# Optimization experiments

Measured on AMD Instinct MI355X. Metric: run time of the kernel, lower is better.

## Reference

```python
import jax, jax.numpy as jnp
import numpy as np

SEQ_LEN = 64  # config.SEQ_LEN
T, B, N, D = 256, 128, 4, 2
H_HIS, H_INT = 32, 8


def _uniform(key, shape, k):
    return jax.random.uniform(key, shape, jnp.float32, -k, k)


def setup_inputs() -> dict:
    key = jax.random.key(0)
    ks = jax.random.split(key, 12)
    kh = 1.0 / np.sqrt(H_HIS)
    ki = 1.0 / np.sqrt(H_INT)
    ko = 1.0 / np.sqrt(40)
    return {
        "inputs": jax.random.normal(ks[0], (T, B, N, D), jnp.float32),
        # history LSTM (input 2 -> hidden 32), gate order i,f,g,o like torch
        "Wih_his": _uniform(ks[1], (4 * H_HIS, D), kh),
        "Whh_his": _uniform(ks[2], (4 * H_HIS, H_HIS), kh),
        "bih_his": _uniform(ks[3], (4 * H_HIS,), kh),
        "bhh_his": _uniform(ks[4], (4 * H_HIS,), kh),
        # interaction LSTM (input 2 -> hidden 8)
        "Wih_int": _uniform(ks[5], (4 * H_INT, D), ki),
        "Whh_int": _uniform(ks[6], (4 * H_INT, H_INT), ki),
        "bih_int": _uniform(ks[7], (4 * H_INT,), ki),
        "bhh_int": _uniform(ks[8], (4 * H_INT,), ki),
        # output Linear(40 -> 2)
        "W_out": _uniform(ks[9], (2, H_HIS + H_INT), ko),
        "b_out": _uniform(ks[10], (2,), ko),
    }


def _lstm_windows(x_w, valid, Wih, Whh, bih, bhh):
    """Run an LSTM over L steps for T independent windows at once.
    x_w: [L, Tw, B, d]  inputs per step (leading padding for short windows)
    valid: [L, Tw] bool; while False the state is held at zero, which is
    exactly equivalent to starting the window fresh at its first valid step.
    Returns final hidden state h: [Tw, B, H].
    """
    H = Whh.shape[1]
    Tw, Bb = x_w.shape[1], x_w.shape[2]
    b = bih + bhh

    def step(carry, xs):
        h, c = carry
        x, v = xs
        g = x @ Wih.T + h @ Whh.T + b            # [Tw, B, 4H]
        i, f, gg, o = jnp.split(g, 4, axis=-1)
        c_new = jax.nn.sigmoid(f) * c + jax.nn.sigmoid(i) * jnp.tanh(gg)
        h_new = jax.nn.sigmoid(o) * jnp.tanh(c_new)
        m = v[:, None, None]
        return (jnp.where(m, h_new, 0.0), jnp.where(m, c_new, 0.0)), None

    init = (jnp.zeros((Tw, Bb, H), x_w.dtype), jnp.zeros((Tw, Bb, H), x_w.dtype))
    (h, _), _ = jax.lax.scan(step, init, (x_w, valid))
    return h


def reference(inputs, Wih_his, Whh_his, bih_his, bhh_his,
              Wih_int, Whh_int, bih_int, bhh_int, W_out, b_out):
    Tt, Bb, Nn, Dd = inputs.shape
    L = SEQ_LEN
    # window index for output frame t: frames t-L+1 .. t (clipped; invalid masked)
    t = jnp.arange(Tt)[:, None]
    s = jnp.arange(L)[None, :]
    idx = t - (L - 1) + s                      # [T, L]
    valid = (idx >= 0)
    idx_c = jnp.clip(idx, 0, Tt - 1)
    x_his = inputs[:, :, -1, :][idx_c]         # [T, L, B, d] (ego / last node)
    x_int = inputs[:, :, 0, :][idx_c]          # [T, L, B, d] (interaction node)
    x_his = jnp.transpose(x_his, (1, 0, 2, 3))  # [L, T, B, d]
    x_int = jnp.transpose(x_int, (1, 0, 2, 3))
    v = jnp.transpose(valid)                   # [L, T]

    h_his = _lstm_windows(x_his, v, Wih_his, Whh_his, bih_his, bhh_his)  # [T,B,32]
    h_int = _lstm_windows(x_int, v, Wih_int, Whh_int, bih_int, bhh_int)  # [T,B,8]
    emb = jnp.concatenate([h_his, h_int], axis=-1)                       # [T,B,40]
    return emb @ W_out.T + b_out                                         # [T,B,2]
```

## Files before the change

kernel.cpp:

```cpp
#include <hip/hip_runtime.h>


typedef float v2f __attribute__((ext_vector_type(2)));
typedef float v4f __attribute__((ext_vector_type(4)));
typedef _Float16 h8v __attribute__((ext_vector_type(8)));

static __device__ __forceinline__ float fexp2(float x) {
    return __builtin_amdgcn_exp2f(x);
}
static __device__ __forceinline__ float frcp(float x) {
    return __builtin_amdgcn_rcpf(x);
}
static __device__ __forceinline__ void pk_fma(v2f& d, v2f a, v2f b) {
    asm("v_pk_fma_f32 %0, %1, %2, %0" : "+v"(d) : "v"(a), "v"(b));
}
static __device__ __forceinline__ v2f loh(v4f v) {
    return __builtin_shufflevector(v, v, 0, 1);
}
static __device__ __forceinline__ v2f hih(v4f v) {
    return __builtin_shufflevector(v, v, 2, 3);
}
static __device__ __forceinline__ unsigned short f2h(float f) {
    _Float16 h = (_Float16)f;
    unsigned short u;
    __builtin_memcpy(&u, &h, 2);
    return u;
}

#define LOG2E    1.442695041f
#define TWOLOG2E 2.885390082f

__global__ __launch_bounds__(256) void prep_kernel(
    const float* __restrict__ Wih_his, const float* __restrict__ Whh_his,
    const float* __restrict__ bih_his, const float* __restrict__ bhh_his,
    const float* __restrict__ Wih_int, const float* __restrict__ Whh_int,
    const float* __restrict__ bih_int, const float* __restrict__ bhh_int,
    float* __restrict__ ws)
{
    const int i = blockIdx.x * 256 + threadIdx.x;
    if (i < 4480) {
        if (i < 256) {
            const int r = i >> 1;
            const float s = (r >= 64 && r < 96) ? -TWOLOG2E : -LOG2E;
            ws[i] = Wih_his[i] * s;
        } else if (i < 384) {
            const int r = i - 256;
            const float s = (r >= 64 && r < 96) ? -TWOLOG2E : -LOG2E;
            ws[i] = (bih_his[r] + bhh_his[r]) * s;
        } else {
            const int e = i - 384, r = e >> 5;
            const float s = (r >= 64 && r < 96) ? -TWOLOG2E : -LOG2E;
            ws[i] = Whh_his[e] * s;
        }
    } else if (i < 4544) {
        const int e = i - 4480, r = e >> 1;
        const float s = (r >= 16 && r < 24) ? -TWOLOG2E : -LOG2E;
        ws[i] = Wih_int[e] * s;
    } else if (i < 4576) {
        const int r = i - 4544;
        const float s = (r >= 16 && r < 24) ? -TWOLOG2E : -LOG2E;
        ws[i] = (bih_int[r] + bhh_int[r]) * s;
    } else if (i < 4832) {
        const int e = i - 4576, r = e >> 3;
        const float s = (r >= 16 && r < 24) ? -TWOLOG2E : -LOG2E;
        ws[i] = Whh_int[e] * s;
    } else if (i < 4960) {
        const int p = i - 4832;
        const int T = p >> 4, n = p & 15;
        const int gi = T >> 1, u = 2 * n + (T & 1);
        const int r = gi * 32 + u;
        const float s = (gi == 2) ? -TWOLOG2E : -LOG2E;
        ws[5120 + p] = (bih_his[r] + bhh_his[r]) * s;
    } else if (i < 5216) {
        const int e = i - 4960;
        const int p = e >> 1, comp = e & 1;
        const int T = p >> 4, n = p & 15;
        const int gi = T >> 1, u = 2 * n + (T & 1);
        const int r = gi * 32 + u;
        const float s = (gi == 2) ? -TWOLOG2E : -LOG2E;
        ws[5376 + e] = Wih_his[r * 2 + comp] * s;
    } else if (i < 9312) {
        const int e = i - 5216;
        const int p = e >> 5, k = e & 31;
        const int T = p >> 4, n = p & 15;
        const int gi = T >> 1, u = 2 * n + (T & 1);
        const int r = gi * 32 + u;
        const float s = (gi == 2) ? -TWOLOG2E : -LOG2E;
        reinterpret_cast<unsigned short*>(ws)[11776 + e] =
            f2h(Whh_his[r * 32 + k] * s);
    }
}

__global__ __launch_bounds__(64) void int_kernel(
    const float* __restrict__ inp, const float* __restrict__ ws,
    const float* __restrict__ W_out, float* __restrict__ eInt)
{
    __shared__ __align__(16) float ib[2][8][8];

    const int lane = threadIdx.x;
    const int W    = blockIdx.x;
    const int t    = W >> 4;
    const int g    = lane >> 3;
    const int u    = lane & 7;
    const int b    = ((W & 15) << 3) | g;
    const int nsteps = (t >= 63) ? 64 : (t + 1);
    const int tau0   = (t >= 63) ? (t - 63) : 0;

    v2f wi[4][4], wxi[4];
    float bi[4];
    {
        const v2f* wsWi = reinterpret_cast<const v2f*>(ws + 4576);
        const v2f* wsXi = reinterpret_cast<const v2f*>(ws + 4480);
#pragma unroll
        for (int q = 0; q < 4; ++q) {
            const v2f* row = wsWi + (q * 8 + u) * 4;
#pragma unroll
            for (int k = 0; k < 4; ++k) wi[q][k] = row[k];
            bi[q]  = ws[4544 + q * 8 + u];
            wxi[q] = wsXi[q * 8 + u];
        }
    }

    ib[0][g][u] = 0.f;
    float cc = 0.f, h = 0.f;

    const float* xc = inp + tau0 * 1024 + b * 8;
    float2 xv2 = *reinterpret_cast<const float2*>(xc);
    xc += 1024;

#pragma unroll 1
    for (int s = 0; s < nsteps; ++s) {
        __builtin_amdgcn_wave_barrier();
        asm volatile("s_waitcnt lgkmcnt(0)" ::: "memory");
        __builtin_amdgcn_wave_barrier();

        const int rb = s & 1, wb = rb ^ 1;
        const v4f* ip = reinterpret_cast<const v4f*>(&ib[rb][g][0]);
        const v4f i0 = ip[0], i1 = ip[1];

        float2 nx = {0.f, 0.f};
        if (s + 1 < nsteps) nx = *reinterpret_cast<const float2*>(xc);
        xc += 1024;
        const v2f xv = {xv2.x, xv2.y};

        float a[4];
#pragma unroll
        for (int q = 0; q < 4; ++q) {
            v2f acc = {bi[q], 0.f};
            pk_fma(acc, wxi[q], xv);
            pk_fma(acc, wi[q][0], loh(i0));
            pk_fma(acc, wi[q][1], hih(i0));
            pk_fma(acc, wi[q][2], loh(i1));
            pk_fma(acc, wi[q][3], hih(i1));
            a[q] = acc.x + acc.y;
        }
        const float si = frcp(1.f + fexp2(a[0]));
        const float sf = frcp(1.f + fexp2(a[1]));
        const float tg = fmaf(2.f, frcp(1.f + fexp2(a[2])), -1.f);
        const float so = frcp(1.f + fexp2(a[3]));
        cc = fmaf(sf, cc, si * tg);
        h = so * fmaf(-2.f, frcp(1.f + fexp2(TWOLOG2E * cc)), 1.f);
        ib[wb][g][u] = h;

        xv2 = nx;
    }

    float e0 = W_out[32 + u] * h;
    float e1 = W_out[72 + u] * h;
#pragma unroll
    for (int m = 4; m >= 1; m >>= 1) {
        e0 += __shfl_xor(e0, m);
        e1 += __shfl_xor(e1, m);
    }
    if (u == 0) {
        float2 o; o.x = e0; o.y = e1;
        reinterpret_cast<float2*>(eInt)[t * 128 + b] = o;
    }
}

__global__ __launch_bounds__(64) void his_kernel(
    const float* __restrict__ inp, const float* __restrict__ ws,
    const float* __restrict__ W_out, const float* __restrict__ b_out,
    const float* __restrict__ eInt, float* __restrict__ out)
{
    __shared__ __align__(16) unsigned short hm[2][16][40];

    const int lane = threadIdx.x;
    const int n    = lane & 15;
    const int quad = lane >> 4;
    const int Wd   = blockIdx.x;
    const int t    = Wd >> 3;
    const int bg   = Wd & 7;
    const int nsteps = (t >= 63) ? 64 : (t + 1);
    const int tau0   = (t >= 63) ? (t - 63) : 0;

    h8v Bf[8];
    {
        const h8v* wb = reinterpret_cast<const h8v*>(
            reinterpret_cast<const unsigned short*>(ws) + 11776);
#pragma unroll
        for (int T = 0; T < 8; ++T) Bf[T] = wb[(T * 16 + n) * 4 + quad];
    }
    float cb[8], cw0[8], cw1[8];
#pragma unroll
    for (int T = 0; T < 8; ++T) {
        const int p = T * 16 + n;
        cb[T]  = ws[5120 + p];
        cw0[T] = ws[5376 + 2 * p];
        cw1[T] = ws[5376 + 2 * p + 1];
    }

    const int bbase = bg * 16 + quad * 4;
    const float* xp = inp + tau0 * 1024 + bbase * 8 + 6;
    float2 xc[4];
#pragma unroll
    for (int r = 0; r < 4; ++r)
        xc[r] = *reinterpret_cast<const float2*>(xp + r * 8);
    xp += 1024;

    h8v Af = {};
    float cs[4][2] = {};
    float h0[4] = {}, h1[4] = {};

#pragma unroll 1
    for (int s = 0; s < nsteps; ++s) {
        float2 xn[4];
        if (s + 1 < nsteps) {
#pragma unroll
            for (int r = 0; r < 4; ++r)
                xn[r] = *reinterpret_cast<const float2*>(xp + r * 8);
        } else {
#pragma unroll
            for (int r = 0; r < 4; ++r) xn[r] = make_float2(0.f, 0.f);
        }
        xp += 1024;

        v4f D[8];
#pragma unroll
        for (int T = 0; T < 8; ++T) {
            v4f C;
#pragma unroll
            for (int r = 0; r < 4; ++r)
                C[r] = fmaf(cw1[T], xc[r].y, fmaf(cw0[T], xc[r].x, cb[T]));
            D[T] = __builtin_amdgcn_mfma_f32_16x16x32_f16(Af, Bf[T], C, 0, 0, 0);
        }

#pragma unroll
        for (int r = 0; r < 4; ++r) {
            {
                const float si = frcp(1.f + fexp2(D[0][r]));
                const float sf = frcp(1.f + fexp2(D[2][r]));
                const float tg = fmaf(2.f, frcp(1.f + fexp2(D[4][r])), -1.f);
                const float so = frcp(1.f + fexp2(D[6][r]));
                const float cn = fmaf(sf, cs[r][0], si * tg);
                cs[r][0] = cn;
                h0[r] = so * fmaf(-2.f, frcp(1.f + fexp2(TWOLOG2E * cn)), 1.f);
            }
            {
                const float si = frcp(1.f + fexp2(D[1][r]));
                const float sf = frcp(1.f + fexp2(D[3][r]));
                const float tg = fmaf(2.f, frcp(1.f + fexp2(D[5][r])), -1.f);
                const float so = frcp(1.f + fexp2(D[7][r]));
                const float cn = fmaf(sf, cs[r][1], si * tg);
                cs[r][1] = cn;
                h1[r] = so * fmaf(-2.f, frcp(1.f + fexp2(TWOLOG2E * cn)), 1.f);
            }
        }

        if (s + 1 < nsteps) {
            const int bf = s & 1;
#pragma unroll
            for (int r = 0; r < 4; ++r) {
                const unsigned pk =
                    ((unsigned)f2h(h1[r]) << 16) | f2h(h0[r]);
                *reinterpret_cast<unsigned*>(&hm[bf][quad * 4 + r][2 * n]) = pk;
            }
            __builtin_amdgcn_wave_barrier();
            asm volatile("s_waitcnt lgkmcnt(0)" ::: "memory");
            __builtin_amdgcn_wave_barrier();
            Af = *reinterpret_cast<const h8v*>(&hm[bf][n][quad * 8]);
        }

#pragma unroll
        for (int r = 0; r < 4; ++r) xc[r] = xn[r];
    }

    const float wo0a = W_out[2 * n],      wo0b = W_out[2 * n + 1];
    const float wo1a = W_out[40 + 2 * n], wo1b = W_out[40 + 2 * n + 1];
    float e0[4], e1[4];
#pragma unroll
    for (int r = 0; r < 4; ++r) {
        e0[r] = fmaf(wo0b, h1[r], wo0a * h0[r]);
        e1[r] = fmaf(wo1b, h1[r], wo1a * h0[r]);
#pragma unroll
        for (int m = 1; m <= 8; m <<= 1) {
            e0[r] += __shfl_xor(e0[r], m);
            e1[r] += __shfl_xor(e1[r], m);
        }
    }
    if (n == 0) {
        const float bo0 = b_out[0], bo1 = b_out[1];
#pragma unroll
        for (int r = 0; r < 4; ++r) {
            const int chain = t * 128 + bbase + r;
            const float2 ei = reinterpret_cast<const float2*>(eInt)[chain];
            float2 o;
            o.x = e0[r] + ei.x + bo0;
            o.y = e1[r] + ei.y + bo1;
            reinterpret_cast<float2*>(out)[chain] = o;
        }
    }
}

extern "C" void kernel_launch(void* const* d_in, const int* in_sizes, int n_in,
                              void* d_out, int out_size, void* d_ws, size_t ws_size,
                              hipStream_t stream) {
    const float* inp     = (const float*)d_in[0];
    const float* Wih_his = (const float*)d_in[1];
    const float* Whh_his = (const float*)d_in[2];
    const float* bih_his = (const float*)d_in[3];
    const float* bhh_his = (const float*)d_in[4];
    const float* Wih_int = (const float*)d_in[5];
    const float* Whh_int = (const float*)d_in[6];
    const float* bih_int = (const float*)d_in[7];
    const float* bhh_int = (const float*)d_in[8];
    const float* W_out   = (const float*)d_in[9];
    const float* b_out   = (const float*)d_in[10];
    float* out  = (float*)d_out;
    float* ws   = (float*)d_ws;
    float* eInt = ws + 8192;

    prep_kernel<<<dim3(37), dim3(256), 0, stream>>>(
        Wih_his, Whh_his, bih_his, bhh_his,
        Wih_int, Whh_int, bih_int, bhh_int, ws);

    int_kernel<<<dim3(4096), dim3(64), 0, stream>>>(inp, ws, W_out, eInt);

    his_kernel<<<dim3(2048), dim3(64), 0, stream>>>(
        inp, ws, W_out, b_out, eInt, out);
}
```

Before: 210.3 us.

## Fuse interaction and history LSTM kernels into one launch with atomic output accumulation

Merges the separate interaction and history LSTM kernels into a single kernel that interleaves block types (one history block per two interaction blocks). The prep kernel now initializes the output with the bias, and both branches accumulate their partial projections into the output with atomicAdd instead of going through an intermediate eInt buffer. This removes a kernel launch and its serialization, and lets the two workloads overlap on the GPU. In exchange it adds atomics and makes the result order-dependent, so float rounding may vary between runs.

```diff
diff --git a/kernel.cpp b/kernel.cpp
--- a/kernel.cpp
+++ b/kernel.cpp
@@ -35,7 +35,8 @@
     const float* __restrict__ bih_his, const float* __restrict__ bhh_his,
     const float* __restrict__ Wih_int, const float* __restrict__ Whh_int,
     const float* __restrict__ bih_int, const float* __restrict__ bhh_int,
-    float* __restrict__ ws)
+    float* __restrict__ ws, const float* __restrict__ b_out,
+    float* __restrict__ out)
 {
     const int i = blockIdx.x * 256 + threadIdx.x;
     if (i < 4480) {
@@ -88,17 +89,21 @@
         const float s = (gi == 2) ? -TWOLOG2E : -LOG2E;
         reinterpret_cast<unsigned short*>(ws)[11776 + e] =
             f2h(Whh_his[r * 32 + k] * s);
-    }
-}
-
-__global__ __launch_bounds__(64) void int_kernel(
+    } else if (i >= 9472) {
+        const int j = i - 9472;
+        float4 v;
+        v.x = b_out[0]; v.y = b_out[1];
+        v.z = b_out[0]; v.w = b_out[1];
+        reinterpret_cast<float4*>(out)[j] = v;
+    }
+}
+
+static __device__ __forceinline__ void int_body(
+    const int W, const int lane,
     const float* __restrict__ inp, const float* __restrict__ ws,
-    const float* __restrict__ W_out, float* __restrict__ eInt)
+    const float* __restrict__ W_out, float* __restrict__ out,
+    float ib[2][8][8])
 {
-    __shared__ __align__(16) float ib[2][8][8];
-
-    const int lane = threadIdx.x;
-    const int W    = blockIdx.x;
     const int t    = W >> 4;
     const int g    = lane >> 3;
     const int u    = lane & 7;
@@ -173,22 +178,20 @@
         e1 += __shfl_xor(e1, m);
     }
     if (u == 0) {
-        float2 o; o.x = e0; o.y = e1;
-        reinterpret_cast<float2*>(eInt)[t * 128 + b] = o;
-    }
-}
-
-__global__ __launch_bounds__(64) void his_kernel(
+        const int chain = t * 128 + b;
+        atomicAdd(&out[2 * chain],     e0);
+        atomicAdd(&out[2 * chain + 1], e1);
+    }
+}
+
+static __device__ __forceinline__ void his_body(
+    const int Wd, const int lane,
     const float* __restrict__ inp, const float* __restrict__ ws,
-    const float* __restrict__ W_out, const float* __restrict__ b_out,
-    const float* __restrict__ eInt, float* __restrict__ out)
+    const float* __restrict__ W_out, float* __restrict__ out,
+    unsigned short hm[2][16][40])
 {
-    __shared__ __align__(16) unsigned short hm[2][16][40];
-
-    const int lane = threadIdx.x;
     const int n    = lane & 15;
     const int quad = lane >> 4;
-    const int Wd   = blockIdx.x;
     const int t    = Wd >> 3;
     const int bg   = Wd & 7;
     const int nsteps = (t >= 63) ? 64 : (t + 1);
@@ -299,16 +302,29 @@
         }
     }
     if (n == 0) {
-        const float bo0 = b_out[0], bo1 = b_out[1];
 #pragma unroll
         for (int r = 0; r < 4; ++r) {
             const int chain = t * 128 + bbase + r;
-            const float2 ei = reinterpret_cast<const float2*>(eInt)[chain];
-            float2 o;
-            o.x = e0[r] + ei.x + bo0;
-            o.y = e1[r] + ei.y + bo1;
-            reinterpret_cast<float2*>(out)[chain] = o;
-        }
+            atomicAdd(&out[2 * chain],     e0[r]);
+            atomicAdd(&out[2 * chain + 1], e1[r]);
+        }
+    }
+}
+
+__global__ __launch_bounds__(64) void lstm_fused(
+    const float* __restrict__ inp, const float* __restrict__ ws,
+    const float* __restrict__ W_out, float* __restrict__ out)
+{
+    __shared__ __align__(16) unsigned short hm[2][16][40];
+    __shared__ __align__(16) float ib[2][8][8];
+
+    const int bid  = blockIdx.x;
+    const int lane = threadIdx.x;
+    const int d3   = bid / 3;
+    if (bid - 3 * d3 == 0) {
+        his_body(d3, lane, inp, ws, W_out, out, hm);
+    } else {
+        int_body(bid - d3 - 1, lane, inp, ws, W_out, out, ib);
     }
 }
 
@@ -328,14 +344,10 @@
     const float* b_out   = (const float*)d_in[10];
     float* out  = (float*)d_out;
     float* ws   = (float*)d_ws;
-    float* eInt = ws + 8192;
-
-    prep_kernel<<<dim3(37), dim3(256), 0, stream>>>(
+
+    prep_kernel<<<dim3(101), dim3(256), 0, stream>>>(
         Wih_his, Whh_his, bih_his, bhh_his,
-        Wih_int, Whh_int, bih_int, bhh_int, ws);
-
-    int_kernel<<<dim3(4096), dim3(64), 0, stream>>>(inp, ws, W_out, eInt);
-
-    his_kernel<<<dim3(2048), dim3(64), 0, stream>>>(
-        inp, ws, W_out, b_out, eInt, out);
-}
+        Wih_int, Whh_int, bih_int, bhh_int, ws, b_out, out);
+
+    lstm_fused<<<dim3(6144), dim3(64), 0, stream>>>(inp, ws, W_out, out);
+}
```

Result: slower. 242.0 us (+15.1%).

## Move interaction LSTM recurrence onto MFMA with split-fp16 weights and state

Applied to the files above, without the earlier changes.

Rewrites the interaction LSTM kernel so the hidden-to-gate product runs as 16x16x32 fp16 MFMA. Each wave now handles 16 batch chains instead of 8, which halves the block count. Weights and hidden state are split into hi/lo fp16 pairs so the product keeps near-fp32 accuracy. The hidden state moves between lanes by shuffles instead of LDS. Prep is extended to lay out and scale the interaction weights in the MFMA-friendly order and drops the old unused layouts.

```diff
diff --git a/kernel.cpp b/kernel.cpp
--- a/kernel.cpp
+++ b/kernel.cpp
@@ -10,21 +10,17 @@
 }
 static __device__ __forceinline__ float frcp(float x) {
     return __builtin_amdgcn_rcpf(x);
-}
-static __device__ __forceinline__ void pk_fma(v2f& d, v2f a, v2f b) {
-    asm("v_pk_fma_f32 %0, %1, %2, %0" : "+v"(d) : "v"(a), "v"(b));
-}
-static __device__ __forceinline__ v2f loh(v4f v) {
-    return __builtin_shufflevector(v, v, 0, 1);
-}
-static __device__ __forceinline__ v2f hih(v4f v) {
-    return __builtin_shufflevector(v, v, 2, 3);
 }
 static __device__ __forceinline__ unsigned short f2h(float f) {
     _Float16 h = (_Float16)f;
     unsigned short u;
     __builtin_memcpy(&u, &h, 2);
     return u;
+}
+static __device__ __forceinline__ float h2f(unsigned short u) {
+    _Float16 h;
+    __builtin_memcpy(&h, &u, 2);
+    return (float)h;
 }
 
 #define LOG2E    1.442695041f
@@ -38,32 +34,7 @@
     float* __restrict__ ws)
 {
     const int i = blockIdx.x * 256 + threadIdx.x;
-    if (i < 4480) {
-        if (i < 256) {
-            const int r = i >> 1;
-            const float s = (r >= 64 && r < 96) ? -TWOLOG2E : -LOG2E;
-            ws[i] = Wih_his[i] * s;
-        } else if (i < 384) {
-            const int r = i - 256;
-            const float s = (r >= 64 && r < 96) ? -TWOLOG2E : -LOG2E;
-            ws[i] = (bih_his[r] + bhh_his[r]) * s;
-        } else {
-            const int e = i - 384, r = e >> 5;
-            const float s = (r >= 64 && r < 96) ? -TWOLOG2E : -LOG2E;
-            ws[i] = Whh_his[e] * s;
-        }
-    } else if (i < 4544) {
-        const int e = i - 4480, r = e >> 1;
-        const float s = (r >= 16 && r < 24) ? -TWOLOG2E : -LOG2E;
-        ws[i] = Wih_int[e] * s;
-    } else if (i < 4576) {
-        const int r = i - 4544;
-        const float s = (r >= 16 && r < 24) ? -TWOLOG2E : -LOG2E;
-        ws[i] = (bih_int[r] + bhh_int[r]) * s;
-    } else if (i < 4832) {
-        const int e = i - 4576, r = e >> 3;
-        const float s = (r >= 16 && r < 24) ? -TWOLOG2E : -LOG2E;
-        ws[i] = Whh_int[e] * s;
+    if (i < 4832) {
     } else if (i < 4960) {
         const int p = i - 4832;
         const int T = p >> 4, n = p & 15;
@@ -88,93 +59,148 @@
         const float s = (gi == 2) ? -TWOLOG2E : -LOG2E;
         reinterpret_cast<unsigned short*>(ws)[11776 + e] =
             f2h(Whh_his[r * 32 + k] * s);
-    }
-}
-
-__global__ __launch_bounds__(64) void int_kernel(
+    } else if (i < 9344) {
+        const int s = i - 9312;
+        const int T = s >> 4, m = s & 15, r = m & 3;
+        const int gate = (4 * T + r) >> 1, unit = 2 * (m >> 2) + (r & 1);
+        const int orig = gate * 8 + unit;
+        const float sc = (gate == 2) ? -TWOLOG2E : -LOG2E;
+        ws[7936 + s] = (bih_int[orig] + bhh_int[orig]) * sc;
+    } else if (i < 9408) {
+        const int e = i - 9344;
+        const int s = e >> 1, comp = e & 1;
+        const int T = s >> 4, m = s & 15, r = m & 3;
+        const int gate = (4 * T + r) >> 1, unit = 2 * (m >> 2) + (r & 1);
+        const int orig = gate * 8 + unit;
+        const float sc = (gate == 2) ? -TWOLOG2E : -LOG2E;
+        ws[7968 + e] = Wih_int[orig * 2 + comp] * sc;
+    } else if (i < 9664) {
+        const int e = i - 9408;
+        const int s = e >> 3, k = e & 7;
+        const int T = s >> 4, m = s & 15, r = m & 3;
+        const int gate = (4 * T + r) >> 1, unit = 2 * (m >> 2) + (r & 1);
+        const int orig = gate * 8 + unit;
+        const float sc = (gate == 2) ? -TWOLOG2E : -LOG2E;
+        const float w = Whh_int[orig * 8 + k] * sc;
+        const unsigned short hi = f2h(w);
+        const unsigned short lo = f2h(w - h2f(hi));
+        reinterpret_cast<unsigned short*>(ws)[16128 + e] = hi;
+        reinterpret_cast<unsigned short*>(ws)[8704 + e]  = lo;
+    }
+}
+
+__global__ __launch_bounds__(64) void intm_kernel(
     const float* __restrict__ inp, const float* __restrict__ ws,
     const float* __restrict__ W_out, float* __restrict__ eInt)
 {
-    __shared__ __align__(16) float ib[2][8][8];
-
     const int lane = threadIdx.x;
-    const int W    = blockIdx.x;
-    const int t    = W >> 4;
-    const int g    = lane >> 3;
-    const int u    = lane & 7;
-    const int b    = ((W & 15) << 3) | g;
+    const int n    = lane & 15;
+    const int q    = lane >> 4;
+    const int Wd   = blockIdx.x;
+    const int t    = Wd >> 3;
+    const int bg   = Wd & 7;
     const int nsteps = (t >= 63) ? 64 : (t + 1);
     const int tau0   = (t >= 63) ? (t - 63) : 0;
 
-    v2f wi[4][4], wxi[4];
-    float bi[4];
+    h8v Ai[2];
     {
-        const v2f* wsWi = reinterpret_cast<const v2f*>(ws + 4576);
-        const v2f* wsXi = reinterpret_cast<const v2f*>(ws + 4480);
-#pragma unroll
-        for (int q = 0; q < 4; ++q) {
-            const v2f* row = wsWi + (q * 8 + u) * 4;
-#pragma unroll
-            for (int k = 0; k < 4; ++k) wi[q][k] = row[k];
-            bi[q]  = ws[4544 + q * 8 + u];
-            wxi[q] = wsXi[q * 8 + u];
-        }
-    }
-
-    ib[0][g][u] = 0.f;
-    float cc = 0.f, h = 0.f;
-
-    const float* xc = inp + tau0 * 1024 + b * 8;
-    float2 xv2 = *reinterpret_cast<const float2*>(xc);
-    xc += 1024;
+        const h8v* wah = reinterpret_cast<const h8v*>(
+            reinterpret_cast<const unsigned short*>(ws) + 16128);
+        const h8v* wal = reinterpret_cast<const h8v*>(
+            reinterpret_cast<const unsigned short*>(ws) + 8704);
+#pragma unroll
+        for (int T = 0; T < 2; ++T) {
+            const h8v vh = wah[T * 16 + n];
+            const h8v vl = wal[T * 16 + n];
+            Ai[T] = (q < 2) ? vh : vl;
+        }
+    }
+
+    float cb[2][4], cw0v[2][4], cw1v[2][4];
+#pragma unroll
+    for (int T = 0; T < 2; ++T)
+#pragma unroll
+        for (int r = 0; r < 4; ++r) {
+            const int s = T * 16 + q * 4 + r;
+            cb[T][r]   = ws[7936 + s];
+            cw0v[T][r] = ws[7968 + 2 * s];
+            cw1v[T][r] = ws[7968 + 2 * s + 1];
+        }
+
+    const int chain = bg * 16 + n;
+    const float* xp = inp + tau0 * 1024 + chain * 8;
+    float2 xv = *reinterpret_cast<const float2*>(xp);
+    float2 x1 = make_float2(0.f, 0.f);
+    if (nsteps > 1) x1 = *reinterpret_cast<const float2*>(xp + 1024);
+    xp += 2048;
+
+    union BU { unsigned u[4]; h8v h; } bf;
+    bf.u[0] = bf.u[1] = bf.u[2] = bf.u[3] = 0;
+
+    float cI0 = 0.f, cI1 = 0.f, h0 = 0.f, h1 = 0.f;
 
 #pragma unroll 1
     for (int s = 0; s < nsteps; ++s) {
-        __builtin_amdgcn_wave_barrier();
-        asm volatile("s_waitcnt lgkmcnt(0)" ::: "memory");
-        __builtin_amdgcn_wave_barrier();
-
-        const int rb = s & 1, wb = rb ^ 1;
-        const v4f* ip = reinterpret_cast<const v4f*>(&ib[rb][g][0]);
-        const v4f i0 = ip[0], i1 = ip[1];
-
-        float2 nx = {0.f, 0.f};
-        if (s + 1 < nsteps) nx = *reinterpret_cast<const float2*>(xc);
-        xc += 1024;
-        const v2f xv = {xv2.x, xv2.y};
-
-        float a[4];
-#pragma unroll
-        for (int q = 0; q < 4; ++q) {
-            v2f acc = {bi[q], 0.f};
-            pk_fma(acc, wxi[q], xv);
-            pk_fma(acc, wi[q][0], loh(i0));
-            pk_fma(acc, wi[q][1], hih(i0));
-            pk_fma(acc, wi[q][2], loh(i1));
-            pk_fma(acc, wi[q][3], hih(i1));
-            a[q] = acc.x + acc.y;
-        }
-        const float si = frcp(1.f + fexp2(a[0]));
-        const float sf = frcp(1.f + fexp2(a[1]));
-        const float tg = fmaf(2.f, frcp(1.f + fexp2(a[2])), -1.f);
-        const float so = frcp(1.f + fexp2(a[3]));
-        cc = fmaf(sf, cc, si * tg);
-        h = so * fmaf(-2.f, frcp(1.f + fexp2(TWOLOG2E * cc)), 1.f);
-        ib[wb][g][u] = h;
-
-        xv2 = nx;
-    }
-
-    float e0 = W_out[32 + u] * h;
-    float e1 = W_out[72 + u] * h;
-#pragma unroll
-    for (int m = 4; m >= 1; m >>= 1) {
-        e0 += __shfl_xor(e0, m);
-        e1 += __shfl_xor(e1, m);
-    }
-    if (u == 0) {
+        float2 x2 = make_float2(0.f, 0.f);
+        if (s + 2 < nsteps)
+            x2 = *reinterpret_cast<const float2*>(xp);
+        xp += 1024;
+
+        v4f C0, C1;
+#pragma unroll
+        for (int r = 0; r < 4; ++r) {
+            C0[r] = fmaf(cw1v[0][r], xv.y, fmaf(cw0v[0][r], xv.x, cb[0][r]));
+            C1[r] = fmaf(cw1v[1][r], xv.y, fmaf(cw0v[1][r], xv.x, cb[1][r]));
+        }
+        const v4f D0 = __builtin_amdgcn_mfma_f32_16x16x32_f16(Ai[0], bf.h, C0, 0, 0, 0);
+        const v4f D1 = __builtin_amdgcn_mfma_f32_16x16x32_f16(Ai[1], bf.h, C1, 0, 0, 0);
+
+        {
+            const float si = frcp(1.f + fexp2(D0[0]));
+            const float sf = frcp(1.f + fexp2(D0[2]));
+            const float tg = fmaf(2.f, frcp(1.f + fexp2(D1[0])), -1.f);
+            const float so = frcp(1.f + fexp2(D1[2]));
+            const float cn = fmaf(sf, cI0, si * tg);
+            cI0 = cn;
+            h0 = so * fmaf(-2.f, frcp(1.f + fexp2(TWOLOG2E * cn)), 1.f);
+        }
+        {
+            const float si = frcp(1.f + fexp2(D0[1]));
+            const float sf = frcp(1.f + fexp2(D0[3]));
+            const float tg = fmaf(2.f, frcp(1.f + fexp2(D1[1])), -1.f);
+            const float so = frcp(1.f + fexp2(D1[3]));
+            const float cn = fmaf(sf, cI1, si * tg);
+            cI1 = cn;
+            h1 = so * fmaf(-2.f, frcp(1.f + fexp2(TWOLOG2E * cn)), 1.f);
+        }
+
+        if (s + 1 < nsteps) {
+            const unsigned short h0h = f2h(h0), h1h = f2h(h1);
+            const float h0l = h0 - h2f(h0h);
+            const float h1l = h1 - h2f(h1h);
+            const unsigned pkh = ((unsigned)h1h << 16) | h0h;
+            const unsigned pkl = ((unsigned)f2h(h1l) << 16) | f2h(h0l);
+#pragma unroll
+            for (int d = 0; d < 4; ++d) {
+                const unsigned uh = (unsigned)__shfl((int)pkh, d * 16 + n);
+                const unsigned ul = (unsigned)__shfl((int)pkl, d * 16 + n);
+                bf.u[d] = (q & 1) ? ul : uh;
+            }
+        }
+
+        xv = x1;
+        x1 = x2;
+    }
+
+    const float wo0a = W_out[32 + 2 * q], wo0b = W_out[33 + 2 * q];
+    const float wo1a = W_out[72 + 2 * q], wo1b = W_out[73 + 2 * q];
+    float e0 = fmaf(wo0b, h1, wo0a * h0);
+    float e1 = fmaf(wo1b, h1, wo1a * h0);
+    e0 += __shfl_xor(e0, 16); e1 += __shfl_xor(e1, 16);
+    e0 += __shfl_xor(e0, 32); e1 += __shfl_xor(e1, 32);
+    if (lane < 16) {
         float2 o; o.x = e0; o.y = e1;
-        reinterpret_cast<float2*>(eInt)[t * 128 + b] = o;
+        reinterpret_cast<float2*>(eInt)[t * 128 + chain] = o;
     }
 }
 
@@ -330,11 +356,11 @@
     float* ws   = (float*)d_ws;
     float* eInt = ws + 8192;
 
-    prep_kernel<<<dim3(37), dim3(256), 0, stream>>>(
+    prep_kernel<<<dim3(38), dim3(256), 0, stream>>>(
         Wih_his, Whh_his, bih_his, bhh_his,
         Wih_int, Whh_int, bih_int, bhh_int, ws);
 
-    int_kernel<<<dim3(4096), dim3(64), 0, stream>>>(inp, ws, W_out, eInt);
+    intm_kernel<<<dim3(2048), dim3(64), 0, stream>>>(inp, ws, W_out, eInt);
 
     his_kernel<<<dim3(2048), dim3(64), 0, stream>>>(
         inp, ws, W_out, b_out, eInt, out);
```

Measured after the change: 197.9 us. 5.9% less time.
